# Kernel optimization log

Hardware: AMD Instinct MI355X
Metric: run time of the kernel (lower is better)

## Reference

```python
import jax, jax.numpy as jnp
import numpy as np

NUM_HEADS = 32
HEAD_DIM = 128
ROPE_DIM = 64
HIDDEN = 4096
C_KV = 512
C_Q = 1536
CACHE_LEN = 4096
BATCH = 4


def _apply_rope(x, positions):
    # x: [B, S, H, R]; interleaved rotate-half RoPE at given absolute positions
    R = x.shape[-1]
    inv_freq = 1.0 / (10000.0 ** (jnp.arange(0, R, 2, dtype=jnp.float32) / R))
    ang = positions[:, None].astype(jnp.float32) * inv_freq[None, :]  # [S, R/2]
    cos = jnp.cos(ang)[None, :, None, :]
    sin = jnp.sin(ang)[None, :, None, :]
    x1, x2 = x[..., 0::2], x[..., 1::2]
    out = jnp.stack([x1 * cos - x2 * sin, x1 * sin + x2 * cos], axis=-1)
    return out.reshape(x.shape).astype(x.dtype)


def setup_inputs() -> dict:
    key = jax.random.key(0)
    ks = jax.random.split(key, 12)
    s = lambda fan: 1.0 / np.sqrt(fan)
    return {
        "hidden_states": jax.random.normal(ks[0], (BATCH, 1, HIDDEN), jnp.float32),
        "mask": jnp.zeros((BATCH, 1, 1, CACHE_LEN + 1), jnp.float32),
        "cached_c_KV": jax.random.normal(ks[1], (BATCH, CACHE_LEN, C_KV), jnp.float32),
        "cached_k_R": jax.random.normal(ks[2], (BATCH, CACHE_LEN, ROPE_DIM), jnp.float32),
        "W_DKV": jax.random.normal(ks[3], (HIDDEN, C_KV), jnp.float32) * s(HIDDEN),
        "W_UK": jax.random.normal(ks[4], (C_KV, NUM_HEADS * HEAD_DIM), jnp.float32) * s(C_KV),
        "W_UV": jax.random.normal(ks[5], (C_KV, NUM_HEADS * HEAD_DIM), jnp.float32) * s(C_KV),
        "W_DQ": jax.random.normal(ks[6], (HIDDEN, C_Q), jnp.float32) * s(HIDDEN),
        "W_UQ": jax.random.normal(ks[7], (C_Q, NUM_HEADS * HEAD_DIM), jnp.float32) * s(C_Q),
        "W_QR": jax.random.normal(ks[8], (C_Q, NUM_HEADS * ROPE_DIM), jnp.float32) * s(C_Q),
        "W_KR": jax.random.normal(ks[9], (HIDDEN, ROPE_DIM), jnp.float32) * s(HIDDEN),
        "W_O": jax.random.normal(ks[10], (NUM_HEADS * HEAD_DIM, HIDDEN), jnp.float32) * s(NUM_HEADS * HEAD_DIM),
    }


def reference(hidden_states, mask, cached_c_KV, cached_k_R,
              W_DKV, W_UK, W_UV, W_DQ, W_UQ, W_QR, W_KR, W_O):
    B = hidden_states.shape[0]
    S_cache = cached_c_KV.shape[1]
    scale = 1.0 / np.sqrt(HEAD_DIM + ROPE_DIM)

    # latent projections for current token
    c_KV = hidden_states @ W_DKV                      # [B,1,C_KV]
    k_C = (c_KV @ W_UK).reshape(B, 1, NUM_HEADS, HEAD_DIM)
    v_C = (c_KV @ W_UV).reshape(B, 1, NUM_HEADS, HEAD_DIM)
    c_Q = hidden_states @ W_DQ                        # [B,1,C_Q]
    q_C = (c_Q @ W_UQ).reshape(B, 1, NUM_HEADS, HEAD_DIM)
    q_R = (c_Q @ W_QR).reshape(B, 1, NUM_HEADS, ROPE_DIM)
    k_R = (hidden_states @ W_KR).reshape(B, 1, 1, ROPE_DIM)

    # RoPE at the current decode position (= cache length)
    pos = jnp.array([S_cache], dtype=jnp.int32)
    q_R = _apply_rope(q_R, pos)
    k_R_cur = _apply_rope(k_R, pos)
    k_R_cur = jnp.broadcast_to(k_R_cur, (B, 1, NUM_HEADS, ROPE_DIM))

    q = jnp.concatenate([q_C, q_R], axis=-1)          # [B,1,H,D+R]
    k_cur = jnp.concatenate([k_C, k_R_cur], axis=-1)  # [B,1,H,D+R]

    # re-up-project cached latents (the expensive MLA decode step)
    cached_k_C = (cached_c_KV @ W_UK).reshape(B, S_cache, NUM_HEADS, HEAD_DIM)
    cached_v_C = (cached_c_KV @ W_UV).reshape(B, S_cache, NUM_HEADS, HEAD_DIM)
    cached_k_R_exp = jnp.broadcast_to(cached_k_R[:, :, None, :],
                                      (B, S_cache, NUM_HEADS, ROPE_DIM))
    cached_k = jnp.concatenate([cached_k_C, cached_k_R_exp], axis=-1)

    k = jnp.concatenate([cached_k, k_cur], axis=1)    # [B,S+1,H,D+R]
    v = jnp.concatenate([cached_v_C, v_C], axis=1)    # [B,S+1,H,D]

    # single-query attention: scores [B,H,1,S+1]
    scores = jnp.einsum('bqhd,bkhd->bhqk', q, k) * scale
    scores = scores + mask * -1e9
    probs = jax.nn.softmax(scores, axis=-1)
    attn = jnp.einsum('bhqk,bkhd->bqhd', probs, v).reshape(B, 1, NUM_HEADS * HEAD_DIM)

    out = attn @ W_O                                  # [B,1,HIDDEN]
    new_cached_c_KV = jnp.concatenate([cached_c_KV, c_KV], axis=1)
    new_cached_k_R = jnp.concatenate([cached_k_R, k_R_cur[:, :, 0, :]], axis=1)
    return out, new_cached_c_KV, new_cached_k_R
```

## Files before the change

kernel.cpp:

```cpp
#include <hip/hip_runtime.h>
#include <math.h>

#define NB 4
#define HID 4096
#define CKV 512
#define CQ 1536
#define NH 32
#define HD 128
#define RD 64
#define SS 4096
#define SK 4097
#define SKP 4100

#define SCALE_F 0.07216878364870322f

#define NP1 64
#define NP2 24
#define NPV 32
#define NUV 16
#define NWO 32

#define KD   576
#define QKB_STR 584
#define PBF_STR 4104
#define TV_STR 40
#define SFS  168
#define PSTR 168

typedef __attribute__((ext_vector_type(8))) short short8v;
typedef __attribute__((ext_vector_type(4))) float f32x4;

enum : int {
  WS_QABS  = 0,
  WS_QROPE = WS_QABS + NB*NH*CKV,
  WS_KROPE = WS_QROPE + NB*NH*RD,
  WS_CKV   = WS_KROPE + NB*RD,
  WS_CQ    = WS_CKV + NB*CKV,
  WS_SCA   = WS_CQ + NB*CQ,
  WS_P1    = WS_SCA + NB*NH*SKP,
  WS_P2    = WS_P1 + NP1*NB*528*4,
  WS_OPART = WS_P2 + NP2*NB*6144,
  WS_UVPART= WS_OPART + NPV*NB*NH*CKV,
  WS_WOPART= WS_UVPART + NUV*NB*HID,
  WS_KVBF  = WS_WOPART + NWO*NB*HID,
  WS_QBF   = WS_KVBF + (NB*SK*KD)/2,
  WS_ML    = WS_QBF + (NB*NH*KD)/2,
  WS_TOTAL = WS_ML + NB*NH*NPV*2
};

__device__ inline void fma4(float4& a, float s, const float4& v) {
  a.x += s*v.x; a.y += s*v.y; a.z += s*v.z; a.w += s*v.w;
}
__device__ inline float dot4(const float4& a, const float4& b) {
  return a.x*b.x + a.y*b.y + a.z*b.z + a.w*b.w;
}
__device__ inline unsigned short f2bf(float f) {
  union { float f; unsigned int u; } v; v.f = f;
  unsigned int r = v.u + 0x7FFFu + ((v.u >> 16) & 1u);
  return (unsigned short)(r >> 16);
}
__device__ inline ushort4 f2bf4(float4 v) {
  ushort4 r; r.x = f2bf(v.x); r.y = f2bf(v.y); r.z = f2bf(v.z); r.w = f2bf(v.w);
  return r;
}
__device__ inline float bf2f(unsigned short u) {
  union { unsigned int u; float f; } v; v.u = ((unsigned int)u) << 16;
  return v.f;
}

__global__ __launch_bounds__(256)
void k_proj1copy(const float* __restrict__ hidden,
                 const float* __restrict__ Wdkv,
                 const float* __restrict__ Wdq,
                 const float* __restrict__ Wkr,
                 float* __restrict__ ws,
                 const float4* __restrict__ src_ckv,
                 const float4* __restrict__ src_kr,
                 float4* __restrict__ dst_ckv,
                 float4* __restrict__ dst_kr) {
  __shared__ float4 red_s[4][NB][64];
  unsigned short* kvbf = (unsigned short*)(ws + WS_KVBF);
  const int bx = blockIdx.x;
  if (bx < 576) {
    const int gx = bx % 9, gy = bx / 9;
    const int lane = threadIdx.x & 63, ksub = threadIdx.x >> 6;
    const int col4 = gx * 64 + lane;
    const int k0 = gy * 64 + ksub * 16;
    const bool valid = col4 < 528;
    float4 acc[NB] = {};
    if (valid) {
      const float* W; int C4, wcol4;
      if (col4 < 128)      { W = Wdkv; C4 = 128; wcol4 = col4; }
      else if (col4 < 512) { W = Wdq;  C4 = 384; wcol4 = col4 - 128; }
      else                 { W = Wkr;  C4 = 16;  wcol4 = col4 - 512; }
      const float4* wp = (const float4*)W + (size_t)k0 * C4 + wcol4;
      #pragma unroll
      for (int i = 0; i < 16; ++i) {
        float4 w4 = wp[(size_t)i * C4];
        #pragma unroll
        for (int b = 0; b < NB; ++b) fma4(acc[b], hidden[b*HID + k0 + i], w4);
      }
    }
    #pragma unroll
    for (int b = 0; b < NB; ++b) red_s[ksub][b][lane] = acc[b];
    __syncthreads();
    if (ksub == 0 && valid) {
      #pragma unroll
      for (int b = 0; b < NB; ++b) {
        float4 s = red_s[0][b][lane];
        #pragma unroll
        for (int j = 1; j < 4; ++j) {
          float4 v = red_s[j][b][lane];
          s.x += v.x; s.y += v.y; s.z += v.z; s.w += v.w;
        }
        *(float4*)(ws + WS_P1 + ((size_t)(gy*NB + b)*528 + col4)*4) = s;
      }
    }
  } else {
    const int bxc = bx - 576;
    if (bxc < 8192) {
      int b = bxc >> 11;
      int idx = (bxc & 2047) * 256 + threadIdx.x;
      float4 v = src_ckv[(size_t)b*(SS*CKV/4) + idx];
      dst_ckv[(size_t)b*(SK*CKV/4) + idx] = v;
      int off = idx * 4;
      int k = off >> 9, c = off & 511;
      *(ushort4*)(kvbf + ((size_t)b*SK + k)*KD + c) = f2bf4(v);
    } else {
      int bx2 = bxc - 8192;
      int b = bx2 >> 8;
      int idx = (bx2 & 255) * 256 + threadIdx.x;
      float4 v = src_kr[(size_t)b*(SS*RD/4) + idx];
      dst_kr[(size_t)b*(SK*RD/4) + idx] = v;
      int off = idx * 4;
      int k = off >> 6, rr = off & 63;
      *(ushort4*)(kvbf + ((size_t)b*SK + k)*KD + 512 + rr) = f2bf4(v);
    }
  }
}

__global__ __launch_bounds__(256)
void k_proj2r1(const float* __restrict__ Wuq,
               const float* __restrict__ Wqr,
               float* __restrict__ ws,
               float* __restrict__ out_ckv,
               float* __restrict__ out_kr) {
  __shared__ float4 red_s[4][NB][64];
  __shared__ float act_s[NB][64];
  unsigned short* kvbf = (unsigned short*)(ws + WS_KVBF);
  const int bx = blockIdx.x;
  const int tid = threadIdx.x;
  if (bx < 576) {
    const int gx = bx % 24, gy = bx / 24;
    {
      const int b = tid >> 6, i = tid & 63;
      const int k = gy * 64 + i;
      const float* base = ws + WS_P1 + (size_t)b*2112 + 512 + k;
      float s = 0.f;
      #pragma unroll 8
      for (int p = 0; p < NP1; ++p) s += base[(size_t)p*NB*2112];
      act_s[b][i] = s;
    }
    __syncthreads();
    const int lane = tid & 63, ksub = tid >> 6;
    const int col4 = gx * 64 + lane;
    const float* W; int C4, wcol4;
    if (col4 < 1024) { W = Wuq; C4 = 1024; wcol4 = col4; }
    else             { W = Wqr; C4 = 512;  wcol4 = col4 - 1024; }
    const float4* wp = (const float4*)W + (size_t)(gy*64 + ksub*16) * C4 + wcol4;
    float4 acc[NB] = {};
    #pragma unroll
    for (int i = 0; i < 16; ++i) {
      float4 w4 = wp[(size_t)i * C4];
      #pragma unroll
      for (int b = 0; b < NB; ++b) fma4(acc[b], act_s[b][ksub*16 + i], w4);
    }
    #pragma unroll
    for (int b = 0; b < NB; ++b) red_s[ksub][b][lane] = acc[b];
    __syncthreads();
    if (ksub == 0) {
      #pragma unroll
      for (int b = 0; b < NB; ++b) {
        float4 s = red_s[0][b][lane];
        #pragma unroll
        for (int j = 1; j < 4; ++j) {
          float4 v = red_s[j][b][lane];
          s.x += v.x; s.y += v.y; s.z += v.z; s.w += v.w;
        }
        *(float4*)(ws + WS_P2 + (size_t)(gy*NB + b)*6144 + col4*4) = s;
      }
    }
  } else {
    const int w = (bx - 576) * 256 + tid;
    if (w >= 528*NB) return;
    const int b = w / 528, col4 = w % 528;
    float4 s = {};
    #pragma unroll 8
    for (int p = 0; p < NP1; ++p) {
      float4 v = *(const float4*)(ws + WS_P1 + ((size_t)(p*NB + b)*528 + col4)*4);
      s.x += v.x; s.y += v.y; s.z += v.z; s.w += v.w;
    }
    if (col4 < 128) {
      *(float4*)(ws + WS_CKV + b*CKV + col4*4) = s;
      *(float4*)(out_ckv + (size_t)b*SK*CKV + (size_t)SS*CKV + col4*4) = s;
      *(ushort4*)(kvbf + ((size_t)b*SK + SS)*KD + col4*4) = f2bf4(s);
    } else if (col4 < 512) {
      *(float4*)(ws + WS_CQ + b*CQ + (col4 - 128)*4) = s;
    } else {
      const int c0 = (col4 - 512) * 4;
      const double LN1E4 = 9.210340371976184;
      int i0 = c0 >> 1;
      double a0 = 4096.0 * exp(-(double)i0 / 32.0 * LN1E4);
      double a1 = 4096.0 * exp(-(double)(i0 + 1) / 32.0 * LN1E4);
      float c0f = (float)cos(a0), s0f = (float)sin(a0);
      float c1f = (float)cos(a1), s1f = (float)sin(a1);
      float4 o;
      o.x = s.x*c0f - s.y*s0f;  o.y = s.x*s0f + s.y*c0f;
      o.z = s.z*c1f - s.w*s1f;  o.w = s.z*s1f + s.w*c1f;
      *(float4*)(ws + WS_KROPE + b*RD + c0) = o;
      *(float4*)(out_kr + (size_t)b*SK*RD + (size_t)SS*RD + c0) = o;
      *(ushort4*)(kvbf + ((size_t)b*SK + SS)*KD + 512 + c0) = f2bf4(o);
    }
  }
}

__global__ __launch_bounds__(256)
void k_absorb_rope(const float* __restrict__ Wuk,
                   float* __restrict__ ws) {
  unsigned short* qbf = (unsigned short*)(ws + WS_QBF);
  const int bid = blockIdx.x, tid = threadIdx.x;
  if (bid < 256) {
    const int h = bid >> 3, cq = bid & 7;
    __shared__ float qc_s[NB][HD];
    __shared__ float part_s[NB][256];
    for (int e = tid; e < NB*HD; e += 256) {
      int b = e >> 7, d = e & 127;
      float v = 0.f;
      #pragma unroll
      for (int p = 0; p < NP2; ++p)
        v += ws[WS_P2 + (size_t)(p*NB + b)*6144 + h*HD + d];
      qc_s[b][d] = v;
    }
    __syncthreads();
    const int c = cq*64 + (tid & 63);
    const int dg = tid >> 6;
    const float4* wrow = (const float4*)(Wuk + (size_t)c*(NH*HD) + h*HD + dg*32);
    float acc[NB] = {0,0,0,0};
    #pragma unroll
    for (int d4 = 0; d4 < 8; ++d4) {
      float4 w4 = wrow[d4];
      #pragma unroll
      for (int b = 0; b < NB; ++b)
        acc[b] += dot4(w4, *(const float4*)&qc_s[b][dg*32 + d4*4]);
    }
    #pragma unroll
    for (int b = 0; b < NB; ++b) part_s[b][tid] = acc[b];
    __syncthreads();
    if (tid < 64) {
      #pragma unroll
      for (int b = 0; b < NB; ++b) {
        float v = (part_s[b][tid] + part_s[b][tid+64] + part_s[b][tid+128] + part_s[b][tid+192]) * SCALE_F;
        ws[WS_QABS + (size_t)(b*NH + h)*CKV + cq*64 + tid] = v;
        qbf[(size_t)(b*NH + h)*KD + cq*64 + tid] = f2bf(v);
      }
    }
  } else {
    const int b = bid - 256;
    const double LN1E4 = 9.210340371976184;
    for (int pid = tid; pid < NH*32; pid += 256) {
      int h = pid >> 5, i = pid & 31;
      float x1 = 0.f, x2 = 0.f;
      #pragma unroll
      for (int p = 0; p < NP2; ++p) {
        const float* base = ws + WS_P2 + (size_t)(p*NB + b)*6144 + 4096 + h*RD + 2*i;
        x1 += base[0]; x2 += base[1];
      }
      double ang = 4096.0 * exp(-(double)i / 32.0 * LN1E4);
      float cs = (float)cos(ang), sn = (float)sin(ang);
      float o0 = (x1*cs - x2*sn) * SCALE_F;
      float o1 = (x1*sn + x2*cs) * SCALE_F;
      ws[WS_QROPE + (b*NH + h)*RD + 2*i]     = o0;
      ws[WS_QROPE + (b*NH + h)*RD + 2*i + 1] = o1;
      qbf[(size_t)(b*NH + h)*KD + 512 + 2*i]     = f2bf(o0);
      qbf[(size_t)(b*NH + h)*KD + 512 + 2*i + 1] = f2bf(o1);
    }
  }
}

__global__ __launch_bounds__(256)
void k_attn(const float* __restrict__ mask, float* __restrict__ ws) {
  __shared__ unsigned short kv_s[32 * QKB_STR];
  __shared__ float S_s[32 * SFS];
  unsigned short* P_s  = kv_s;
  unsigned short* kvT_s = kv_s + 32*PSTR;
  const unsigned short* kvbf = (const unsigned short*)(ws + WS_KVBF);
  const unsigned short* qbf  = (const unsigned short*)(ws + WS_QBF);
  const int tid = threadIdx.x;
  const int j  = blockIdx.x;
  const int qy = blockIdx.y;
  const int b  = blockIdx.z;
  const int k0 = j * 128;
  const int NSUB = (j == NPV-1) ? 5 : 4;
  const int wid = tid >> 6, lane = tid & 63;
  const int l15 = lane & 15, lq = lane >> 4;

  const int m0 = (wid & 1) * 16;
  const int n0 = (wid >> 1) * 16;
  const unsigned short* arow = qbf + (size_t)(b*NH + m0 + l15)*KD + lq*8;
  for (int sc = 0; sc < NSUB; ++sc) {
    {
      const int r = tid >> 3, u0 = tid & 7;
      const int k = k0 + sc*32 + r;
      const unsigned short* ksrc = (k <= SS) ? (kvbf + ((size_t)b*SK + k)*KD) : nullptr;
      #pragma unroll
      for (int u8 = 0; u8 < 9; ++u8) {
        int u = (u0 + 8*u8) * 8;
        uint4 kvv = {0u, 0u, 0u, 0u};
        if (ksrc) kvv = *(const uint4*)(ksrc + u);
        *(uint4*)&kv_s[r*QKB_STR + u] = kvv;
      }
    }
    __syncthreads();
    const unsigned short* brow = &kv_s[(n0 + l15)*QKB_STR + lq*8];
    f32x4 acc = {0.f, 0.f, 0.f, 0.f};
    #pragma unroll
    for (int ks = 0; ks < 18; ++ks) {
      short8v a = *(const short8v*)(arow + ks*32);
      short8v bb = *(const short8v*)(brow + ks*32);
      acc = __builtin_amdgcn_mfma_f32_16x16x32_bf16(a, bb, acc, 0, 0, 0);
    }
    const int kk = sc*32 + n0 + l15;
    const bool vkey = (k0 + kk) <= SS;
    #pragma unroll
    for (int r = 0; r < 4; ++r)
      S_s[(m0 + lq*4 + r)*SFS + kk] = vkey ? acc[r] : -1e30f;
    __syncthreads();
  }

  {
    const int row = tid >> 3, i8 = tid & 7;
    const int NK = NSUB * 32;
    float m = -INFINITY;
    for (int kk = i8; kk < NK; kk += 8) {
      int kgl = k0 + kk;
      float mv = (kgl < SK) ? mask[(size_t)b*SK + kgl] : 0.f;
      float v = S_s[row*SFS + kk] + mv * (-1e9f);
      S_s[row*SFS + kk] = v;
      m = fmaxf(m, v);
    }
    m = fmaxf(m, __shfl_xor(m, 1));
    m = fmaxf(m, __shfl_xor(m, 2));
    m = fmaxf(m, __shfl_xor(m, 4));
    float l = 0.f;
    for (int kk = i8; kk < NK; kk += 8) {
      float e = __expf(S_s[row*SFS + kk] - m);
      l += e;
      P_s[row*PSTR + kk] = f2bf(e);
    }
    l += __shfl_xor(l, 1);
    l += __shfl_xor(l, 2);
    l += __shfl_xor(l, 4);
    if (i8 == 0 && qy == 0) {
      float* ml = ws + WS_ML + ((size_t)(b*NH + row)*NPV + j)*2;
      ml[0] = m; ml[1] = l;
    }
  }
  __syncthreads();

  const int c0 = qy * 128;
  f32x4 acc4[4] = {{0,0,0,0},{0,0,0,0},{0,0,0,0},{0,0,0,0}};
  const int kk_st = tid & 31, cgrp = tid >> 5;
  for (int sc = 0; sc < NSUB; ++sc) {
    {
      const int k = k0 + sc*32 + kk_st;
      ushort4 v0 = {0,0,0,0}, v1 = {0,0,0,0}, v2 = {0,0,0,0}, v3 = {0,0,0,0};
      if (k <= SS) {
        const unsigned short* src = kvbf + ((size_t)b*SK + k)*KD + c0 + cgrp*16;
        v0 = *(const ushort4*)(src);
        v1 = *(const ushort4*)(src + 4);
        v2 = *(const ushort4*)(src + 8);
        v3 = *(const ushort4*)(src + 12);
      }
      int cb = cgrp*16;
      kvT_s[(cb+ 0)*TV_STR + kk_st] = v0.x;
      kvT_s[(cb+ 1)*TV_STR + kk_st] = v0.y;
      kvT_s[(cb+ 2)*TV_STR + kk_st] = v0.z;
      kvT_s[(cb+ 3)*TV_STR + kk_st] = v0.w;
      kvT_s[(cb+ 4)*TV_STR + kk_st] = v1.x;
      kvT_s[(cb+ 5)*TV_STR + kk_st] = v1.y;
      kvT_s[(cb+ 6)*TV_STR + kk_st] = v1.z;
      kvT_s[(cb+ 7)*TV_STR + kk_st] = v1.w;
      kvT_s[(cb+ 8)*TV_STR + kk_st] = v2.x;
      kvT_s[(cb+ 9)*TV_STR + kk_st] = v2.y;
      kvT_s[(cb+10)*TV_STR + kk_st] = v2.z;
      kvT_s[(cb+11)*TV_STR + kk_st] = v2.w;
      kvT_s[(cb+12)*TV_STR + kk_st] = v3.x;
      kvT_s[(cb+13)*TV_STR + kk_st] = v3.y;
      kvT_s[(cb+14)*TV_STR + kk_st] = v3.z;
      kvT_s[(cb+15)*TV_STR + kk_st] = v3.w;
    }
    __syncthreads();
    short8v a = *(const short8v*)(&P_s[(m0 + l15)*PSTR + sc*32 + lq*8]);
    #pragma unroll
    for (int t = 0; t < 4; ++t) {
      const int nt = (wid >> 1) + 2*t;
      const unsigned short* brow = &kvT_s[(nt*16 + l15)*TV_STR + lq*8];
      short8v bb = *(const short8v*)(brow);
      acc4[t] = __builtin_amdgcn_mfma_f32_16x16x32_bf16(a, bb, acc4[t], 0, 0, 0);
    }
    __syncthreads();
  }
  #pragma unroll
  for (int t = 0; t < 4; ++t) {
    const int nt = (wid >> 1) + 2*t;
    const int c = c0 + nt*16 + l15;
    #pragma unroll
    for (int r = 0; r < 4; ++r) {
      int h = m0 + lq*4 + r;
      ws[WS_OPART + (((size_t)j*NB + b)*NH + h)*CKV + c] = acc4[t][r];
    }
  }
}

__global__ __launch_bounds__(256)
void k_uv2(const float* __restrict__ Wuv, float* __restrict__ ws) {
  __shared__ float4 red_s[4][NB][64];
  __shared__ float ol_s[NB][2][32];
  const int tid = threadIdx.x;
  const int x = blockIdx.x & 15, y = blockIdx.x >> 4;
  {
    const int b = tid >> 6, hh = (tid >> 5) & 1, ci = tid & 31;
    const int h = 2*x + hh, c = y*32 + ci;
    const float* ml = ws + WS_ML + (size_t)(b*NH + h)*NPV*2;
    float M = -INFINITY;
    #pragma unroll 8
    for (int p = 0; p < NPV; ++p) M = fmaxf(M, ml[p*2]);
    const float* base = ws + WS_OPART + ((size_t)b*NH + h)*CKV + c;
    float s = 0.f, L = 0.f;
    #pragma unroll 4
    for (int p = 0; p < NPV; ++p) {
      float w = __expf(ml[p*2] - M);
      L += w * ml[p*2 + 1];
      s += w * base[(size_t)p*(NB*NH*CKV)];
    }
    ol_s[b][hh][ci] = s / L;
  }
  __syncthreads();
  const int lane = tid & 63, csub = tid >> 6;
  const int col4 = x * 64 + lane;
  const int hh = (col4 >> 5) & 1;
  const float4* wp = (const float4*)Wuv + (size_t)(y*32 + csub*8) * 1024 + col4;
  float4 acc[NB] = {};
  #pragma unroll
  for (int i = 0; i < 8; ++i) {
    float4 w4 = wp[(size_t)i * 1024];
    #pragma unroll
    for (int b = 0; b < NB; ++b)
      fma4(acc[b], ol_s[b][hh][csub*8 + i], w4);
  }
  #pragma unroll
  for (int b = 0; b < NB; ++b) red_s[csub][b][lane] = acc[b];
  __syncthreads();
  if (csub == 0) {
    #pragma unroll
    for (int b = 0; b < NB; ++b) {
      float4 s = red_s[0][b][lane];
      #pragma unroll
      for (int j = 1; j < 4; ++j) {
        float4 v = red_s[j][b][lane];
        s.x += v.x; s.y += v.y; s.z += v.z; s.w += v.w;
      }
      *(float4*)(ws + WS_UVPART + (size_t)(y*NB + b)*HID + col4*4) = s;
    }
  }
}

__global__ __launch_bounds__(256)
void k_wo2(const float* __restrict__ Wo, float* __restrict__ ws) {
  __shared__ float4 red_s[4][NB][64];
  __shared__ float at_s[NB][128];
  const int tid = threadIdx.x;
  const int x = blockIdx.x & 15, y = blockIdx.x >> 4;
  {
    const int b = tid >> 6, q = tid & 63;
    #pragma unroll
    for (int e = 0; e < 2; ++e) {
      int idx = q*2 + e;
      const float* base = ws + WS_UVPART + (size_t)b*HID + y*128 + idx;
      float s = 0.f;
      #pragma unroll
      for (int p = 0; p < NUV; ++p) s += base[(size_t)p*(NB*HID)];
      at_s[b][idx] = s;
    }
  }
  __syncthreads();
  const int lane = tid & 63, ksub = tid >> 6;
  const int col4 = x * 64 + lane;
  const float4* wp = (const float4*)Wo + (size_t)(y*128 + ksub*32) * 1024 + col4;
  float4 acc[NB] = {};
  #pragma unroll 8
  for (int i = 0; i < 32; ++i) {
    float4 w4 = wp[(size_t)i * 1024];
    #pragma unroll
    for (int b = 0; b < NB; ++b)
      fma4(acc[b], at_s[b][ksub*32 + i], w4);
  }
  #pragma unroll
  for (int b = 0; b < NB; ++b) red_s[ksub][b][lane] = acc[b];
  __syncthreads();
  if (ksub == 0) {
    #pragma unroll
    for (int b = 0; b < NB; ++b) {
      float4 s = red_s[0][b][lane];
      #pragma unroll
      for (int j = 1; j < 4; ++j) {
        float4 v = red_s[j][b][lane];
        s.x += v.x; s.y += v.y; s.z += v.z; s.w += v.w;
      }
      *(float4*)(ws + WS_WOPART + (size_t)(y*NB + b)*HID + col4*4) = s;
    }
  }
}

__global__ __launch_bounds__(256)
void k_reduce5(const float* __restrict__ ws, float* __restrict__ out) {
  const int idx = blockIdx.x * 256 + threadIdx.x;
  float4 s = {};
  #pragma unroll 8
  for (int p = 0; p < NWO; ++p) {
    float4 v = *(const float4*)(ws + WS_WOPART + (size_t)p*(NB*HID) + (size_t)idx*4);
    s.x += v.x; s.y += v.y; s.z += v.z; s.w += v.w;
  }
  *(float4*)(out + (size_t)idx*4) = s;
}

extern "C" void kernel_launch(void* const* d_in, const int* in_sizes, int n_in,
                              void* d_out, int out_size, void* d_ws, size_t ws_size,
                              hipStream_t stream) {
  (void)in_sizes; (void)n_in; (void)out_size; (void)ws_size;
  const float* hidden = (const float*)d_in[0];
  const float* mask   = (const float*)d_in[1];
  const float* ckv_c  = (const float*)d_in[2];
  const float* kr_c   = (const float*)d_in[3];
  const float* Wdkv   = (const float*)d_in[4];
  const float* Wuk    = (const float*)d_in[5];
  const float* Wuv    = (const float*)d_in[6];
  const float* Wdq    = (const float*)d_in[7];
  const float* Wuq    = (const float*)d_in[8];
  const float* Wqr    = (const float*)d_in[9];
  const float* Wkr    = (const float*)d_in[10];
  const float* Wo     = (const float*)d_in[11];
  float* out = (float*)d_out;
  float* ws  = (float*)d_ws;
  float* out_ckv = out + NB*HID;
  float* out_kr  = out + NB*HID + (size_t)NB*SK*CKV;

  k_proj1copy<<<9792, 256, 0, stream>>>(hidden, Wdkv, Wdq, Wkr, ws,
                                        (const float4*)ckv_c, (const float4*)kr_c,
                                        (float4*)out_ckv, (float4*)out_kr);
  k_proj2r1<<<585, 256, 0, stream>>>(Wuq, Wqr, ws, out_ckv, out_kr);
  k_absorb_rope<<<260, 256, 0, stream>>>(Wuk, ws);
  k_attn<<<dim3(NPV, 4, 4), 256, 0, stream>>>(mask, ws);
  k_uv2<<<256, 256, 0, stream>>>(Wuv, ws);
  k_wo2<<<512, 256, 0, stream>>>(Wo, ws);
  k_reduce5<<<16, 256, 0, stream>>>(ws, out);
}
```

Baseline: 120.5 us.

## Split fused attention into separate score MFMA kernel and PV flash kernel

The fused attention kernel is split in two. A new score kernel computes QK^T scores with MFMA over 32-key tiles on a 129x4 grid and writes them to a global scratch buffer. A second kernel reads those scores, applies the mask and softmax, and does the PV product. In the old kernel each of the 4 qy blocks recomputed the same scores, so the split removes that redundant QK work and the serial K-tile loop per block, at the cost of an extra launch and a global round-trip for the scores.

```diff
diff --git a/kernel.cpp b/kernel.cpp
--- a/kernel.cpp
+++ b/kernel.cpp
@@ -22,7 +22,6 @@
 
 #define KD   576
 #define QKB_STR 584
-#define PBF_STR 4104
 #define TV_STR 40
 #define SFS  168
 #define PSTR 168
@@ -288,63 +287,74 @@
 }
 
 __global__ __launch_bounds__(256)
-void k_attn(const float* __restrict__ mask, float* __restrict__ ws) {
+void k_scores_mfma(float* __restrict__ ws) {
   __shared__ unsigned short kv_s[32 * QKB_STR];
-  __shared__ float S_s[32 * SFS];
-  unsigned short* P_s  = kv_s;
-  unsigned short* kvT_s = kv_s + 32*PSTR;
   const unsigned short* kvbf = (const unsigned short*)(ws + WS_KVBF);
   const unsigned short* qbf  = (const unsigned short*)(ws + WS_QBF);
+  const int tid = threadIdx.x;
+  const int b  = blockIdx.y;
+  const int k0 = blockIdx.x * 32;
+  {
+    const int r = tid >> 3, u0 = tid & 7;
+    const int k = k0 + r;
+    const unsigned short* ksrc = (k <= SS) ? (kvbf + ((size_t)b*SK + k)*KD) : nullptr;
+    #pragma unroll
+    for (int j = 0; j < 9; ++j) {
+      int u = (u0 + 8*j) * 8;
+      uint4 kvv = {0u, 0u, 0u, 0u};
+      if (ksrc) kvv = *(const uint4*)(ksrc + u);
+      *(uint4*)&kv_s[r*QKB_STR + u] = kvv;
+    }
+  }
+  __syncthreads();
+  const int wid = tid >> 6, lane = tid & 63;
+  const int m0 = (wid & 1) * 16;
+  const int n0 = (wid >> 1) * 16;
+  const int l15 = lane & 15, lq = lane >> 4;
+  const unsigned short* arow = qbf + (size_t)(b*NH + m0 + l15)*KD + lq*8;
+  const unsigned short* brow = &kv_s[(n0 + l15)*QKB_STR + lq*8];
+  f32x4 acc = {0.f, 0.f, 0.f, 0.f};
+  #pragma unroll
+  for (int ks = 0; ks < 18; ++ks) {
+    short8v a = *(const short8v*)(arow + ks*32);
+    short8v bb = *(const short8v*)(brow + ks*32);
+    acc = __builtin_amdgcn_mfma_f32_16x16x32_bf16(a, bb, acc, 0, 0, 0);
+  }
+  const int key = k0 + n0 + l15;
+  if (key <= SS) {
+    #pragma unroll
+    for (int r = 0; r < 4; ++r) {
+      int h = m0 + lq*4 + r;
+      ws[WS_SCA + (size_t)(b*NH + h)*SKP + key] = acc[r];
+    }
+  }
+}
+
+__global__ __launch_bounds__(256)
+void k_pvflash(const float* __restrict__ mask, float* __restrict__ ws) {
+  __shared__ float S_s[32 * SFS];
+  __shared__ unsigned short P_s[32 * PSTR];
+  __shared__ unsigned short kvT_s[128 * TV_STR];
+  const unsigned short* kvbf = (const unsigned short*)(ws + WS_KVBF);
   const int tid = threadIdx.x;
   const int j  = blockIdx.x;
   const int qy = blockIdx.y;
   const int b  = blockIdx.z;
   const int k0 = j * 128;
   const int NSUB = (j == NPV-1) ? 5 : 4;
+  const int NK = NSUB * 32;
   const int wid = tid >> 6, lane = tid & 63;
   const int l15 = lane & 15, lq = lane >> 4;
-
   const int m0 = (wid & 1) * 16;
-  const int n0 = (wid >> 1) * 16;
-  const unsigned short* arow = qbf + (size_t)(b*NH + m0 + l15)*KD + lq*8;
-  for (int sc = 0; sc < NSUB; ++sc) {
-    {
-      const int r = tid >> 3, u0 = tid & 7;
-      const int k = k0 + sc*32 + r;
-      const unsigned short* ksrc = (k <= SS) ? (kvbf + ((size_t)b*SK + k)*KD) : nullptr;
-      #pragma unroll
-      for (int u8 = 0; u8 < 9; ++u8) {
-        int u = (u0 + 8*u8) * 8;
-        uint4 kvv = {0u, 0u, 0u, 0u};
-        if (ksrc) kvv = *(const uint4*)(ksrc + u);
-        *(uint4*)&kv_s[r*QKB_STR + u] = kvv;
-      }
-    }
-    __syncthreads();
-    const unsigned short* brow = &kv_s[(n0 + l15)*QKB_STR + lq*8];
-    f32x4 acc = {0.f, 0.f, 0.f, 0.f};
-    #pragma unroll
-    for (int ks = 0; ks < 18; ++ks) {
-      short8v a = *(const short8v*)(arow + ks*32);
-      short8v bb = *(const short8v*)(brow + ks*32);
-      acc = __builtin_amdgcn_mfma_f32_16x16x32_bf16(a, bb, acc, 0, 0, 0);
-    }
-    const int kk = sc*32 + n0 + l15;
-    const bool vkey = (k0 + kk) <= SS;
-    #pragma unroll
-    for (int r = 0; r < 4; ++r)
-      S_s[(m0 + lq*4 + r)*SFS + kk] = vkey ? acc[r] : -1e30f;
-    __syncthreads();
-  }
 
   {
     const int row = tid >> 3, i8 = tid & 7;
-    const int NK = NSUB * 32;
+    const float* srow = ws + WS_SCA + (size_t)(b*NH + row)*SKP;
+    const float* mrow = mask + (size_t)b*SK;
     float m = -INFINITY;
     for (int kk = i8; kk < NK; kk += 8) {
       int kgl = k0 + kk;
-      float mv = (kgl < SK) ? mask[(size_t)b*SK + kgl] : 0.f;
-      float v = S_s[row*SFS + kk] + mv * (-1e9f);
+      float v = (kgl < SK) ? (srow[kgl] + mrow[kgl] * (-1e9f)) : -1e30f;
       S_s[row*SFS + kk] = v;
       m = fmaxf(m, v);
     }
@@ -560,7 +570,8 @@
                                         (float4*)out_ckv, (float4*)out_kr);
   k_proj2r1<<<585, 256, 0, stream>>>(Wuq, Wqr, ws, out_ckv, out_kr);
   k_absorb_rope<<<260, 256, 0, stream>>>(Wuk, ws);
-  k_attn<<<dim3(NPV, 4, 4), 256, 0, stream>>>(mask, ws);
+  k_scores_mfma<<<dim3(129, 4), 256, 0, stream>>>(ws);
+  k_pvflash<<<dim3(NPV, 4, 4), 256, 0, stream>>>(mask, ws);
   k_uv2<<<256, 256, 0, stream>>>(Wuv, ws);
   k_wo2<<<512, 256, 0, stream>>>(Wo, ws);
   k_reduce5<<<16, 256, 0, stream>>>(ws, out);
```

Measured after the change: 107.1 us. -11.1%, faster.
